# Performance work log

Measured on AMD Instinct MI355X. Metric: run time of the kernel, lower is better.

## Reference

```python
import jax, jax.numpy as jnp
import numpy as np

EPS = 1e-20

def setup_inputs() -> dict:
    key = jax.random.key(0)
    k1, k2 = jax.random.split(key)
    x = jax.random.normal(k1, (8192, 4096), dtype=jnp.float32)
    weight = jax.random.normal(k2, (4096, 4096), dtype=jnp.float32)  # [out, in]
    return {"x": x, "weight": weight}

def reference(x, weight):
    # Binarize activations and weights with sign(v + eps), then matmul.
    xb = jnp.sign(x + EPS)
    wb = jnp.sign(weight + EPS)
    return jnp.matmul(xb, wb.T)  # [N, out]
```

## Files before the change

kernel.cpp:

```cpp
#include <hip/hip_runtime.h>
#include <stdint.h>

#define EPSF 1e-20f

typedef __attribute__((ext_vector_type(4))) int i32x4;
typedef __attribute__((ext_vector_type(16))) int i32x16;


__global__ __launch_bounds__(256)
void bin_i8_kernel(const float4* __restrict__ src, uint32_t* __restrict__ dst,
                   int n4) {
    int base = blockIdx.x * 1024 + threadIdx.x;
#pragma unroll
    for (int j = 0; j < 4; ++j) {
        int idx = base + j * 256;
        if (idx < n4) {
            float4 v = src[idx];
            uint32_t b0 = (v.x < -EPSF) ? 0xFFu : 0x01u;
            uint32_t b1 = (v.y < -EPSF) ? 0xFFu : 0x01u;
            uint32_t b2 = (v.z < -EPSF) ? 0xFFu : 0x01u;
            uint32_t b3 = (v.w < -EPSF) ? 0xFFu : 0x01u;
            dst[idx] = b0 | (b1 << 8) | (b2 << 16) | (b3 << 24);
        }
    }
}

#define GM 128
#define GN 128
#define GK 128

__global__ __launch_bounds__(256, 3)
void i8mfma_gemm(const char* __restrict__ xi8, const char* __restrict__ wi8,
                 float* __restrict__ out) {
    __shared__ char xs[GM * GK];
    __shared__ char wsh[GN * GK];

    const int t = threadIdx.x;
    const int lane = t & 63;
    const int wave = t >> 6;
    const int wm = (wave >> 1) * 64;
    const int wn = (wave & 1) * 64;
    const int row0 = blockIdx.y * GM;
    const int col0 = blockIdx.x * GN;
    const int lrow = lane & 31;
    const int half = lane >> 5;

    i32x16 acc[2][2];
#pragma unroll
    for (int r = 0; r < 2; ++r)
#pragma unroll
        for (int c = 0; c < 2; ++c)
#pragma unroll
            for (int e = 0; e < 16; ++e) acc[r][c][e] = 0;

    for (int kc = 0; kc < 4096; kc += GK) {
        __syncthreads();
#pragma unroll
        for (int j = 0; j < 4; ++j) {
            int c = j * 256 + t;
            int row = c >> 3;
            int q = c & 7;
            int qg = q ^ (row & 7);
            const char* srcx = xi8 + (size_t)(row0 + row) * 4096 + kc + qg * 16;
            __builtin_amdgcn_global_load_lds((const uint32_t*)srcx,
                                             (uint32_t*)(xs + c * 16), 16, 0, 0);
            const char* srcw = wi8 + (size_t)(col0 + row) * 4096 + kc + qg * 16;
            __builtin_amdgcn_global_load_lds((const uint32_t*)srcw,
                                             (uint32_t*)(wsh + c * 16), 16, 0, 0);
        }
        __syncthreads();

#pragma unroll
        for (int s = 0; s < 4; ++s) {
            int g = 2 * s + half;
            i32x4 a[2], b[2];
#pragma unroll
            for (int r = 0; r < 2; ++r) {
                int row = wm + r * 32 + lrow;
                int qs = g ^ (row & 7);
                a[r] = *(const i32x4*)(xs + row * GK + qs * 16);
            }
#pragma unroll
            for (int c = 0; c < 2; ++c) {
                int col = wn + c * 32 + lrow;
                int qs = g ^ (col & 7);
                b[c] = *(const i32x4*)(wsh + col * GK + qs * 16);
            }
#pragma unroll
            for (int r = 0; r < 2; ++r)
#pragma unroll
                for (int c = 0; c < 2; ++c)
                    acc[r][c] = __builtin_amdgcn_mfma_i32_32x32x32_i8(
                        a[r], b[c], acc[r][c], 0, 0, 0);
        }
    }

#pragma unroll
    for (int r = 0; r < 2; ++r)
#pragma unroll
        for (int c = 0; c < 2; ++c)
#pragma unroll
            for (int e = 0; e < 16; ++e) {
                int rr = row0 + wm + r * 32 + (e & 3) + 8 * (e >> 2) + 4 * half;
                int cc = col0 + wn + c * 32 + lrow;
                out[(size_t)rr * 4096 + cc] = (float)acc[r][c][e];
            }
}


__global__ __launch_bounds__(256)
void binarize_kernel(const float* __restrict__ src,
                     unsigned long long* __restrict__ dst, int n256) {
    int wave = blockIdx.x * 4 + (threadIdx.x >> 6);
    if (wave >= n256) return;
    int lane = threadIdx.x & 63;
    const float4* p = (const float4*)(src + (size_t)wave * 256);
    float4 v = p[lane];
    unsigned long long m0 = __ballot(v.x < -EPSF);
    unsigned long long m1 = __ballot(v.y < -EPSF);
    unsigned long long m2 = __ballot(v.z < -EPSF);
    unsigned long long m3 = __ballot(v.w < -EPSF);
    if (lane < 4) {
        unsigned long long m = (lane == 0) ? m0 : (lane == 1) ? m1
                             : (lane == 2) ? m2 : m3;
        dst[(size_t)wave * 4 + lane] = m;
    }
}

#define BM 128
#define BN 128
#define CHUNK_Q 8
#define NCHUNK 4
#define LDSS 9

__global__ __launch_bounds__(256, 2)
void bingemm_kernel(const uint4* __restrict__ xb, const uint4* __restrict__ wb,
                    float* __restrict__ out) {
    __shared__ uint4 xsl[BM * LDSS];
    __shared__ uint4 wsl[BN * LDSS];

    const int t  = threadIdx.x;
    const int tx = t & 15;
    const int ty = t >> 4;
    const int row0 = blockIdx.y * BM;
    const int col0 = blockIdx.x * BN;

    int acc[8][8];
#pragma unroll
    for (int a = 0; a < 8; ++a)
#pragma unroll
        for (int b = 0; b < 8; ++b) acc[a][b] = 0;

    const int srow = t >> 3;
    const int sq   = t & 7;

    for (int c = 0; c < NCHUNK; ++c) {
        __syncthreads();
#pragma unroll
        for (int k = 0; k < 4; ++k) {
            int r = srow + 32 * k;
            xsl[r * LDSS + sq] = xb[(size_t)(row0 + r) * 32 + c * CHUNK_Q + sq];
            wsl[r * LDSS + sq] = wb[(size_t)(col0 + r) * 32 + c * CHUNK_Q + sq];
        }
        __syncthreads();

#pragma unroll
        for (int q = 0; q < CHUNK_Q; ++q) {
            uint4 xq[8], wq[8];
#pragma unroll
            for (int ri = 0; ri < 8; ++ri)
                xq[ri] = xsl[(ty + 16 * ri) * LDSS + q];
#pragma unroll
            for (int cj = 0; cj < 8; ++cj)
                wq[cj] = wsl[(tx + 16 * cj) * LDSS + q];
#pragma unroll
            for (int ri = 0; ri < 8; ++ri)
#pragma unroll
                for (int cj = 0; cj < 8; ++cj) {
                    acc[ri][cj] += __builtin_popcount(xq[ri].x ^ wq[cj].x);
                    acc[ri][cj] += __builtin_popcount(xq[ri].y ^ wq[cj].y);
                    acc[ri][cj] += __builtin_popcount(xq[ri].z ^ wq[cj].z);
                    acc[ri][cj] += __builtin_popcount(xq[ri].w ^ wq[cj].w);
                }
        }
    }

#pragma unroll
    for (int ri = 0; ri < 8; ++ri) {
        size_t i = row0 + ty + 16 * ri;
#pragma unroll
        for (int cj = 0; cj < 8; ++cj) {
            int j = col0 + tx + 16 * cj;
            out[i * 4096 + j] = (float)(4096 - 2 * acc[ri][cj]);
        }
    }
}

extern "C" void kernel_launch(void* const* d_in, const int* in_sizes, int n_in,
                              void* d_out, int out_size, void* d_ws, size_t ws_size,
                              hipStream_t stream) {
    const float* x = (const float*)d_in[0];
    const float* w = (const float*)d_in[1];
    float* out = (float*)d_out;

    const int M = 8192, N = 4096, K = 4096;
    const size_t need_i8 = (size_t)M * K + (size_t)N * K;

    if (ws_size >= need_i8) {
        char* xi8 = (char*)d_ws;
        char* wi8 = xi8 + (size_t)M * K;

        int n4x = (M * K) / 4;
        int n4w = (N * K) / 4;
        bin_i8_kernel<<<n4x / 1024, 256, 0, stream>>>(
            (const float4*)x, (uint32_t*)xi8, n4x);
        bin_i8_kernel<<<n4w / 1024, 256, 0, stream>>>(
            (const float4*)w, (uint32_t*)wi8, n4w);

        dim3 grid(N / GN, M / GM);
        i8mfma_gemm<<<grid, 256, 0, stream>>>(xi8, wi8, out);
    } else {
        uint32_t* xbits = (uint32_t*)d_ws;
        uint32_t* wbits = xbits + (size_t)M * (K / 32);

        binarize_kernel<<<(M * K) / 1024, 256, 0, stream>>>(
            x, (unsigned long long*)xbits, (M * K) / 256);
        binarize_kernel<<<(N * K) / 1024, 256, 0, stream>>>(
            w, (unsigned long long*)wbits, (N * K) / 256);

        dim3 grid(N / BN, M / BM);
        bingemm_kernel<<<grid, 256, 0, stream>>>(
            (const uint4*)xbits, (const uint4*)wbits, out);
    }
}
```

Before: 389.8 us.

## Enlarge int8 MFMA GEMM tile to 256x128 and fuse binarize launches

Result: no change. 395.1 us (+1.4%).

```diff
diff --git a/kernel.cpp b/kernel.cpp
--- a/kernel.cpp
+++ b/kernel.cpp
@@ -6,90 +6,99 @@
 typedef __attribute__((ext_vector_type(4))) int i32x4;
 typedef __attribute__((ext_vector_type(16))) int i32x16;
 
-
 __global__ __launch_bounds__(256)
-void bin_i8_kernel(const float4* __restrict__ src, uint32_t* __restrict__ dst,
-                   int n4) {
-    int base = blockIdx.x * 1024 + threadIdx.x;
-#pragma unroll
-    for (int j = 0; j < 4; ++j) {
+void bin_i8_kernel(const float4* __restrict__ xsrc, const float4* __restrict__ wsrc,
+                   uint32_t* __restrict__ xdst, uint32_t* __restrict__ wdst,
+                   int nblk_x) {
+    const float4* src;
+    uint32_t* dst;
+    int base;
+    if (blockIdx.x < (unsigned)nblk_x) {
+        src = xsrc; dst = xdst; base = blockIdx.x * 2048 + threadIdx.x;
+    } else {
+        src = wsrc; dst = wdst; base = (blockIdx.x - nblk_x) * 2048 + threadIdx.x;
+    }
+#pragma unroll
+    for (int j = 0; j < 8; ++j) {
         int idx = base + j * 256;
-        if (idx < n4) {
-            float4 v = src[idx];
-            uint32_t b0 = (v.x < -EPSF) ? 0xFFu : 0x01u;
-            uint32_t b1 = (v.y < -EPSF) ? 0xFFu : 0x01u;
-            uint32_t b2 = (v.z < -EPSF) ? 0xFFu : 0x01u;
-            uint32_t b3 = (v.w < -EPSF) ? 0xFFu : 0x01u;
-            dst[idx] = b0 | (b1 << 8) | (b2 << 16) | (b3 << 24);
-        }
-    }
-}
-
-#define GM 128
+        float4 v = src[idx];
+        uint32_t b0 = (v.x < -EPSF) ? 0xFFu : 0x01u;
+        uint32_t b1 = (v.y < -EPSF) ? 0xFFu : 0x01u;
+        uint32_t b2 = (v.z < -EPSF) ? 0xFFu : 0x01u;
+        uint32_t b3 = (v.w < -EPSF) ? 0xFFu : 0x01u;
+        dst[idx] = b0 | (b1 << 8) | (b2 << 16) | (b3 << 24);
+    }
+}
+
+#define GM 256
 #define GN 128
-#define GK 128
-
-__global__ __launch_bounds__(256, 3)
+#define GKB 128
+
+__global__ __launch_bounds__(256, 2)
 void i8mfma_gemm(const char* __restrict__ xi8, const char* __restrict__ wi8,
                  float* __restrict__ out) {
-    __shared__ char xs[GM * GK];
-    __shared__ char wsh[GN * GK];
+    __shared__ char xs[GM * GKB];
+    __shared__ char wsh[GN * GKB];
 
     const int t = threadIdx.x;
     const int lane = t & 63;
     const int wave = t >> 6;
-    const int wm = (wave >> 1) * 64;
-    const int wn = (wave & 1) * 64;
+    const int lrow = lane & 31;
+    const int half = lane >> 5;
     const int row0 = blockIdx.y * GM;
     const int col0 = blockIdx.x * GN;
-    const int lrow = lane & 31;
-    const int half = lane >> 5;
-
-    i32x16 acc[2][2];
+    const int wm = wave * 64;
+
+    i32x16 acc[2][4];
 #pragma unroll
     for (int r = 0; r < 2; ++r)
 #pragma unroll
-        for (int c = 0; c < 2; ++c)
+        for (int c = 0; c < 4; ++c)
 #pragma unroll
             for (int e = 0; e < 16; ++e) acc[r][c][e] = 0;
 
-    for (int kc = 0; kc < 4096; kc += GK) {
-        __syncthreads();
+    for (int kc = 0; kc < 4096; kc += GKB) {
+        __syncthreads();
+#pragma unroll
+        for (int j = 0; j < 8; ++j) {
+            int c = j * 256 + t;
+            int row = c >> 3;
+            int qg = (c & 7) ^ (row & 7);
+            __builtin_amdgcn_global_load_lds(
+                (const uint32_t*)(xi8 + (size_t)(row0 + row) * 4096 + kc + qg * 16),
+                (uint32_t*)(xs + c * 16), 16, 0, 0);
+        }
 #pragma unroll
         for (int j = 0; j < 4; ++j) {
             int c = j * 256 + t;
             int row = c >> 3;
-            int q = c & 7;
-            int qg = q ^ (row & 7);
-            const char* srcx = xi8 + (size_t)(row0 + row) * 4096 + kc + qg * 16;
-            __builtin_amdgcn_global_load_lds((const uint32_t*)srcx,
-                                             (uint32_t*)(xs + c * 16), 16, 0, 0);
-            const char* srcw = wi8 + (size_t)(col0 + row) * 4096 + kc + qg * 16;
-            __builtin_amdgcn_global_load_lds((const uint32_t*)srcw,
-                                             (uint32_t*)(wsh + c * 16), 16, 0, 0);
+            int qg = (c & 7) ^ (row & 7);
+            __builtin_amdgcn_global_load_lds(
+                (const uint32_t*)(wi8 + (size_t)(col0 + row) * 4096 + kc + qg * 16),
+                (uint32_t*)(wsh + c * 16), 16, 0, 0);
         }
         __syncthreads();
 
 #pragma unroll
         for (int s = 0; s < 4; ++s) {
             int g = 2 * s + half;
-            i32x4 a[2], b[2];
+            i32x4 a[2], b[4];
 #pragma unroll
             for (int r = 0; r < 2; ++r) {
                 int row = wm + r * 32 + lrow;
                 int qs = g ^ (row & 7);
-                a[r] = *(const i32x4*)(xs + row * GK + qs * 16);
+                a[r] = *(const i32x4*)(xs + row * GKB + qs * 16);
             }
 #pragma unroll
-            for (int c = 0; c < 2; ++c) {
-                int col = wn + c * 32 + lrow;
+            for (int c = 0; c < 4; ++c) {
+                int col = c * 32 + lrow;
                 int qs = g ^ (col & 7);
-                b[c] = *(const i32x4*)(wsh + col * GK + qs * 16);
+                b[c] = *(const i32x4*)(wsh + col * GKB + qs * 16);
             }
 #pragma unroll
             for (int r = 0; r < 2; ++r)
 #pragma unroll
-                for (int c = 0; c < 2; ++c)
+                for (int c = 0; c < 4; ++c)
                     acc[r][c] = __builtin_amdgcn_mfma_i32_32x32x32_i8(
                         a[r], b[c], acc[r][c], 0, 0, 0);
         }
@@ -98,15 +107,14 @@
 #pragma unroll
     for (int r = 0; r < 2; ++r)
 #pragma unroll
-        for (int c = 0; c < 2; ++c)
+        for (int c = 0; c < 4; ++c)
 #pragma unroll
             for (int e = 0; e < 16; ++e) {
                 int rr = row0 + wm + r * 32 + (e & 3) + 8 * (e >> 2) + 4 * half;
-                int cc = col0 + wn + c * 32 + lrow;
+                int cc = col0 + c * 32 + lrow;
                 out[(size_t)rr * 4096 + cc] = (float)acc[r][c][e];
             }
 }
-
 
 __global__ __launch_bounds__(256)
 void binarize_kernel(const float* __restrict__ src,
@@ -129,8 +137,6 @@
 
 #define BM 128
 #define BN 128
-#define CHUNK_Q 8
-#define NCHUNK 4
 #define LDSS 9
 
 __global__ __launch_bounds__(256, 2)
@@ -138,41 +144,30 @@
                     float* __restrict__ out) {
     __shared__ uint4 xsl[BM * LDSS];
     __shared__ uint4 wsl[BN * LDSS];
-
-    const int t  = threadIdx.x;
-    const int tx = t & 15;
-    const int ty = t >> 4;
-    const int row0 = blockIdx.y * BM;
-    const int col0 = blockIdx.x * BN;
-
+    const int t = threadIdx.x, tx = t & 15, ty = t >> 4;
+    const int row0 = blockIdx.y * BM, col0 = blockIdx.x * BN;
     int acc[8][8];
 #pragma unroll
     for (int a = 0; a < 8; ++a)
 #pragma unroll
         for (int b = 0; b < 8; ++b) acc[a][b] = 0;
-
-    const int srow = t >> 3;
-    const int sq   = t & 7;
-
-    for (int c = 0; c < NCHUNK; ++c) {
+    const int srow = t >> 3, sq = t & 7;
+    for (int c = 0; c < 4; ++c) {
         __syncthreads();
 #pragma unroll
         for (int k = 0; k < 4; ++k) {
             int r = srow + 32 * k;
-            xsl[r * LDSS + sq] = xb[(size_t)(row0 + r) * 32 + c * CHUNK_Q + sq];
-            wsl[r * LDSS + sq] = wb[(size_t)(col0 + r) * 32 + c * CHUNK_Q + sq];
-        }
-        __syncthreads();
-
-#pragma unroll
-        for (int q = 0; q < CHUNK_Q; ++q) {
+            xsl[r * LDSS + sq] = xb[(size_t)(row0 + r) * 32 + c * 8 + sq];
+            wsl[r * LDSS + sq] = wb[(size_t)(col0 + r) * 32 + c * 8 + sq];
+        }
+        __syncthreads();
+#pragma unroll
+        for (int q = 0; q < 8; ++q) {
             uint4 xq[8], wq[8];
 #pragma unroll
-            for (int ri = 0; ri < 8; ++ri)
-                xq[ri] = xsl[(ty + 16 * ri) * LDSS + q];
-#pragma unroll
-            for (int cj = 0; cj < 8; ++cj)
-                wq[cj] = wsl[(tx + 16 * cj) * LDSS + q];
+            for (int ri = 0; ri < 8; ++ri) xq[ri] = xsl[(ty + 16 * ri) * LDSS + q];
+#pragma unroll
+            for (int cj = 0; cj < 8; ++cj) wq[cj] = wsl[(tx + 16 * cj) * LDSS + q];
 #pragma unroll
             for (int ri = 0; ri < 8; ++ri)
 #pragma unroll
@@ -184,15 +179,12 @@
                 }
         }
     }
-
 #pragma unroll
     for (int ri = 0; ri < 8; ++ri) {
         size_t i = row0 + ty + 16 * ri;
 #pragma unroll
-        for (int cj = 0; cj < 8; ++cj) {
-            int j = col0 + tx + 16 * cj;
-            out[i * 4096 + j] = (float)(4096 - 2 * acc[ri][cj]);
-        }
+        for (int cj = 0; cj < 8; ++cj)
+            out[i * 4096 + col0 + tx + 16 * cj] = (float)(4096 - 2 * acc[ri][cj]);
     }
 }
 
@@ -210,24 +202,21 @@
         char* xi8 = (char*)d_ws;
         char* wi8 = xi8 + (size_t)M * K;
 
-        int n4x = (M * K) / 4;
-        int n4w = (N * K) / 4;
-        bin_i8_kernel<<<n4x / 1024, 256, 0, stream>>>(
-            (const float4*)x, (uint32_t*)xi8, n4x);
-        bin_i8_kernel<<<n4w / 1024, 256, 0, stream>>>(
-            (const float4*)w, (uint32_t*)wi8, n4w);
+        int nblk_x = (M * K) / (4 * 2048);
+        int nblk_w = (N * K) / (4 * 2048);
+        bin_i8_kernel<<<nblk_x + nblk_w, 256, 0, stream>>>(
+            (const float4*)x, (const float4*)w,
+            (uint32_t*)xi8, (uint32_t*)wi8, nblk_x);
 
         dim3 grid(N / GN, M / GM);
         i8mfma_gemm<<<grid, 256, 0, stream>>>(xi8, wi8, out);
     } else {
         uint32_t* xbits = (uint32_t*)d_ws;
         uint32_t* wbits = xbits + (size_t)M * (K / 32);
-
         binarize_kernel<<<(M * K) / 1024, 256, 0, stream>>>(
             x, (unsigned long long*)xbits, (M * K) / 256);
         binarize_kernel<<<(N * K) / 1024, 256, 0, stream>>>(
             w, (unsigned long long*)wbits, (N * K) / 256);
-
         dim3 grid(N / BN, M / BM);
         bingemm_kernel<<<grid, 256, 0, stream>>>(
             (const uint4*)xbits, (const uint4*)wbits, out);
```
